# Kernel tuning notes

Hardware: AMD Instinct MI355X
Metric: run time of the kernel (lower is better)

Reference implementation:

```python
import jax, jax.numpy as jnp
import numpy as np

EMBED_DIM = 1024
NUM_HEADS = 16
HEAD_DIM = EMBED_DIM // NUM_HEADS


def setup_inputs() -> dict:
    key = jax.random.key(0)
    ks = jax.random.split(key, 12)
    B, S, D = 4, 2048, EMBED_DIM
    scale = 1.0 / np.sqrt(D)
    inp = {
        "query": jax.random.normal(ks[0], (B, S, D), jnp.float32),
        "key": jax.random.normal(ks[1], (B, S, D), jnp.float32),
        "value": jax.random.normal(ks[2], (B, S, D), jnp.float32),
        # nn.Linear weights: [out_features, in_features], y = x @ W.T + b
        "Wq": jax.random.normal(ks[3], (D, D), jnp.float32) * scale,
        "bq": jnp.zeros((D,), jnp.float32),
        "Wk": jax.random.normal(ks[4], (D, D), jnp.float32) * scale,
        "bk": jnp.zeros((D,), jnp.float32),
        "Wv": jax.random.normal(ks[5], (D, D), jnp.float32) * scale,
        "bv": jnp.zeros((D,), jnp.float32),
        "Wo": jax.random.normal(ks[6], (D, D), jnp.float32) * scale,
        "bo": jnp.zeros((D,), jnp.float32),
    }
    return inp


def reference(query, key, value, Wq, bq, Wk, bk, Wv, bv, Wo, bo):
    B, Sq, D = query.shape
    Sk = key.shape[1]
    H, Dh = NUM_HEADS, HEAD_DIM

    def proj(x, W, b):
        # [B,S,D] -> [B,H,S,Dh]
        y = jnp.einsum('bsd,ed->bse', x, W) + b
        return y.reshape(x.shape[0], x.shape[1], H, Dh).transpose(0, 2, 1, 3)

    q = proj(query, Wq, bq)
    k = proj(key, Wk, bk)
    v = proj(value, Wv, bv)

    # sigmoid attention (no softmax); dropout is identity in eval mode
    scores = jnp.einsum('bhqd,bhkd->bhqk', q, k) / jnp.sqrt(jnp.float32(Dh)).astype(q.dtype)
    attn = jax.nn.sigmoid(scores)
    out = jnp.einsum('bhqk,bhkd->bhqd', attn, v)

    out = out.transpose(0, 2, 1, 3).reshape(B, Sq, D)
    return jnp.einsum('bsd,ed->bse', out, Wo) + bo
```

## Files before the change

kernel.cpp:

```cpp
#include <hip/hip_runtime.h>


typedef _Float16 f16x2 __attribute__((ext_vector_type(2)));
typedef _Float16 f16x4 __attribute__((ext_vector_type(4)));
typedef _Float16 f16x8 __attribute__((ext_vector_type(8)));
typedef __fp16   h16x2 __attribute__((ext_vector_type(2)));
typedef float    f32x4 __attribute__((ext_vector_type(4)));
typedef float    f32x16 __attribute__((ext_vector_type(16)));

typedef __attribute__((address_space(3))) void* lds_vp;
typedef const __attribute__((address_space(1))) void* gbl_vp;

__device__ __forceinline__ void gld_lds16(const void* g, void* l) {
  __builtin_amdgcn_global_load_lds((gbl_vp)g, (lds_vp)l, 16, 0, 0);
}

__device__ __forceinline__ f16x8 cvt8(float4 a, float4 b) {
  return (f16x8){(_Float16)a.x, (_Float16)a.y, (_Float16)a.z, (_Float16)a.w,
                 (_Float16)b.x, (_Float16)b.y, (_Float16)b.z, (_Float16)b.w};
}

__device__ __forceinline__ f16x2 pk2(float a, float b) {
  h16x2 r = __builtin_amdgcn_cvt_pkrtz(a, b);
  return __builtin_bit_cast(f16x2, r);
}

__device__ __forceinline__ float exp2_fast(float x) {
#if __has_builtin(__builtin_amdgcn_exp2f)
  return __builtin_amdgcn_exp2f(x);
#else
  float r;
  asm("v_exp_f32 %0, %1" : "=v"(r) : "v"(x));
  return r;
#endif
}

#define BM 128
#define BN 128
#define BK 32

template <bool AF16, bool BF16, bool TRANSV, bool OUTF32>
__global__ __launch_bounds__(256) void gemm_bt(const void* __restrict__ Av,
                                               const void* __restrict__ Bv,
                                               const float* __restrict__ bias,
                                               void* __restrict__ Yv,
                                               int M, int N, int K) {
  __shared__ __align__(16) _Float16 sA[BM * BK];
  __shared__ __align__(16) _Float16 sB[BN * BK];

  const int t = threadIdx.x, lane = t & 63, wid = t >> 6;
  const int m0 = blockIdx.x * BM, n0 = blockIdx.y * BN;
  const int wm = (wid >> 1) * 64, wn = (wid & 1) * 64;
  const int lrow = lane & 15, g = lane >> 4;

  f32x4 acc[4][4] = {};

  const int arow = 16 * wid + (lane >> 2);
  const int gq = (lane & 3) ^ ((lane >> 3) & 3);
  _Float16* lA1 = sA + wid * 512;
  _Float16* lA2 = sA + 2048 + wid * 512;
  _Float16* lB1 = sB + wid * 512;
  _Float16* lB2 = sB + 2048 + wid * 512;

  const int mrow = t >> 1, mhalf = t & 1;
  const int mm = (mrow >> 1) & 3;
  const int ch_lo = mrow * 4 + ((2 * mhalf) ^ mm);
  const int ch_hi = ch_lo ^ 1;

  const _Float16* pA16a = nullptr; const _Float16* pA16b = nullptr;
  const float* pA32 = nullptr;
  if constexpr (AF16) {
    const _Float16* A = (const _Float16*)Av;
    pA16a = A + (size_t)(m0 + arow) * K + gq * 8;
    pA16b = A + (size_t)(m0 + 64 + arow) * K + gq * 8;
  } else {
    pA32 = (const float*)Av + (size_t)(m0 + mrow) * K + mhalf * 16;
  }
  const _Float16* pB16a = nullptr; const _Float16* pB16b = nullptr;
  const float* pB32 = nullptr;
  if constexpr (BF16) {
    const _Float16* B = (const _Float16*)Bv;
    pB16a = B + (size_t)(n0 + arow) * K + gq * 8;
    pB16b = B + (size_t)(n0 + 64 + arow) * K + gq * 8;
  } else {
    pB32 = (const float*)Bv + (size_t)(n0 + mrow) * K + mhalf * 16;
  }

  const int xr = g ^ ((lrow >> 1) & 3);

  for (int k0 = 0; k0 < K; k0 += BK) {
    float4 av[4], bv4[4];
    if constexpr (!AF16) {
      const float4* p = (const float4*)(pA32 + k0);
      av[0] = p[0]; av[1] = p[1]; av[2] = p[2]; av[3] = p[3];
    }
    if constexpr (!BF16) {
      const float4* p = (const float4*)(pB32 + k0);
      bv4[0] = p[0]; bv4[1] = p[1]; bv4[2] = p[2]; bv4[3] = p[3];
    }
    __syncthreads();
    if constexpr (AF16) {
      gld_lds16(pA16a + k0, lA1);
      gld_lds16(pA16b + k0, lA2);
    } else {
      *(f16x8*)(sA + ch_lo * 8) = cvt8(av[0], av[1]);
      *(f16x8*)(sA + ch_hi * 8) = cvt8(av[2], av[3]);
    }
    if constexpr (BF16) {
      gld_lds16(pB16a + k0, lB1);
      gld_lds16(pB16b + k0, lB2);
    } else {
      *(f16x8*)(sB + ch_lo * 8) = cvt8(bv4[0], bv4[1]);
      *(f16x8*)(sB + ch_hi * 8) = cvt8(bv4[2], bv4[3]);
    }
    __syncthreads();

    f16x8 af[4], bf[4];
#pragma unroll
    for (int i = 0; i < 4; i++)
      af[i] = *(const f16x8*)(sA + (wm + i * 16 + lrow) * 32 + xr * 8);
#pragma unroll
    for (int j = 0; j < 4; j++)
      bf[j] = *(const f16x8*)(sB + (wn + j * 16 + lrow) * 32 + xr * 8);
#pragma unroll
    for (int i = 0; i < 4; i++)
#pragma unroll
      for (int j = 0; j < 4; j++)
        acc[i][j] = __builtin_amdgcn_mfma_f32_16x16x32_f16(af[i], bf[j], acc[i][j], 0, 0, 0);
  }

  const int orow = g * 4, ocol = lrow;
#pragma unroll
  for (int j = 0; j < 4; j++) {
    const int col = n0 + wn + j * 16 + ocol;
    const float bv = bias[col];
#pragma unroll
    for (int i = 0; i < 4; i++) {
      const int row = m0 + wm + i * 16 + orow;
      if constexpr (TRANSV) {
        _Float16* VT = (_Float16*)Yv;
        int s = row & 2047;
        int sp = (s & ~12) | ((s & 4) << 1) | ((s & 8) >> 1);
        _Float16* dst = VT + (((size_t)(row >> 11) * 16 + (col >> 6)) * 64 + (col & 63)) * 2048 + sp;
        f16x4 v = {(_Float16)(acc[i][j][0] + bv), (_Float16)(acc[i][j][1] + bv),
                   (_Float16)(acc[i][j][2] + bv), (_Float16)(acc[i][j][3] + bv)};
        *(f16x4*)dst = v;
      } else if constexpr (OUTF32) {
        float* Y = (float*)Yv;
#pragma unroll
        for (int r = 0; r < 4; r++) Y[(size_t)(row + r) * N + col] = acc[i][j][r] + bv;
      } else {
        _Float16* Y = (_Float16*)Yv;
#pragma unroll
        for (int r = 0; r < 4; r++) Y[(size_t)(row + r) * N + col] = (_Float16)(acc[i][j][r] + bv);
      }
    }
  }
}

__global__ __launch_bounds__(256) void qkv_gemm(const _Float16* __restrict__ Xq,
                                                const _Float16* __restrict__ Xk,
                                                const _Float16* __restrict__ Xv,
                                                const _Float16* __restrict__ W,
                                                const float* __restrict__ bq,
                                                const float* __restrict__ bk,
                                                const float* __restrict__ bv,
                                                _Float16* __restrict__ Qo,
                                                _Float16* __restrict__ Ko,
                                                _Float16* __restrict__ VT) {
  __shared__ __align__(16) _Float16 sA[BM * BK];
  __shared__ __align__(16) _Float16 sB[BN * BK];

  const int t = threadIdx.x, lane = t & 63, wid = t >> 6;
  const int n0g = blockIdx.x * BN, m0 = blockIdx.y * BM;
  const int seg = blockIdx.x >> 3, n0 = n0g & 1023;
  const _Float16* A = (seg == 0) ? Xq : (seg == 1) ? Xk : Xv;
  const float* bias = (seg == 0) ? bq : (seg == 1) ? bk : bv;
  const int K = 1024;

  const int wm = (wid >> 1) * 64, wn = (wid & 1) * 64;
  const int lrow = lane & 15, g = lane >> 4;

  f32x4 acc[4][4] = {};

  const int arow = 16 * wid + (lane >> 2);
  const int gq = (lane & 3) ^ ((lane >> 3) & 3);
  _Float16* lA1 = sA + wid * 512;
  _Float16* lA2 = sA + 2048 + wid * 512;
  _Float16* lB1 = sB + wid * 512;
  _Float16* lB2 = sB + 2048 + wid * 512;

  const _Float16* pA16a = A + (size_t)(m0 + arow) * K + gq * 8;
  const _Float16* pA16b = A + (size_t)(m0 + 64 + arow) * K + gq * 8;
  const _Float16* pB16a = W + (size_t)(n0g + arow) * K + gq * 8;
  const _Float16* pB16b = W + (size_t)(n0g + 64 + arow) * K + gq * 8;

  const int xr = g ^ ((lrow >> 1) & 3);

  for (int k0 = 0; k0 < K; k0 += BK) {
    __syncthreads();
    gld_lds16(pA16a + k0, lA1);
    gld_lds16(pA16b + k0, lA2);
    gld_lds16(pB16a + k0, lB1);
    gld_lds16(pB16b + k0, lB2);
    __syncthreads();

    f16x8 af[4], bf[4];
#pragma unroll
    for (int i = 0; i < 4; i++)
      af[i] = *(const f16x8*)(sA + (wm + i * 16 + lrow) * 32 + xr * 8);
#pragma unroll
    for (int j = 0; j < 4; j++)
      bf[j] = *(const f16x8*)(sB + (wn + j * 16 + lrow) * 32 + xr * 8);
#pragma unroll
    for (int i = 0; i < 4; i++)
#pragma unroll
      for (int j = 0; j < 4; j++)
        acc[i][j] = __builtin_amdgcn_mfma_f32_16x16x32_f16(af[i], bf[j], acc[i][j], 0, 0, 0);
  }

  const int orow = g * 4, ocol = lrow;
#pragma unroll
  for (int j = 0; j < 4; j++) {
    const int col = n0 + wn + j * 16 + ocol;
    const float bvv = bias[col];
#pragma unroll
    for (int i = 0; i < 4; i++) {
      const int row = m0 + wm + i * 16 + orow;
      if (seg == 2) {
        int s = row & 2047;
        int sp = (s & ~12) | ((s & 4) << 1) | ((s & 8) >> 1);
        _Float16* dst = VT + (((size_t)(row >> 11) * 16 + (col >> 6)) * 64 + (col & 63)) * 2048 + sp;
        f16x4 v = {(_Float16)(acc[i][j][0] + bvv), (_Float16)(acc[i][j][1] + bvv),
                   (_Float16)(acc[i][j][2] + bvv), (_Float16)(acc[i][j][3] + bvv)};
        *(f16x4*)dst = v;
      } else {
        _Float16* Y = (seg == 0) ? Qo : Ko;
#pragma unroll
        for (int r = 0; r < 4; r++) Y[(size_t)(row + r) * 1024 + col] = (_Float16)(acc[i][j][r] + bvv);
      }
    }
  }
}

#define LDS_ROW 72
#define TILE_E (64 * LDS_ROW)

__global__ __launch_bounds__(256, 3) void attn_sig(const _Float16* __restrict__ Q,
                                                   const _Float16* __restrict__ K,
                                                   const _Float16* __restrict__ VT,
                                                   _Float16* __restrict__ O) {
  __shared__ __align__(16) _Float16 smem[4 * TILE_E];

  const int t = threadIdx.x, lane = t & 63, wid = t >> 6;
  const int l31 = lane & 31, g5 = lane >> 5;
  const int b = blockIdx.z, h = blockIdx.y, q0 = blockIdx.x * 128;
  const int qw = q0 + wid * 32;
  const int NT = 32;

  f16x8 qf[4];
  {
    const _Float16* qp = Q + (size_t)(b * 2048 + qw + l31) * 1024 + h * 64;
#pragma unroll
    for (int dhc = 0; dhc < 4; dhc++)
      qf[dhc] = *(const f16x8*)(qp + dhc * 16 + g5 * 8) * (_Float16)-0.18033688f;
  }

  f32x16 oacc[2] = {};

  const int srow = t >> 2, scol = (t & 3) * 16;
  const _Float16* kbase = K + ((size_t)(b * 2048) + srow) * 1024 + h * 64 + scol;
  const _Float16* vbase = VT + ((size_t)((b * 16 + h) * 64 + srow)) * 2048 + scol;

#define LOAD_TILE(tile)                                                  \
  ka = *(const uint4*)(kbase + (size_t)(tile) * 64 * 1024);              \
  kb = *(const uint4*)(kbase + (size_t)(tile) * 64 * 1024 + 8);          \
  va = *(const uint4*)(vbase + (tile) * 64);                             \
  vb = *(const uint4*)(vbase + (tile) * 64 + 8);

#define WRITE_TILE(p)                                                    \
  {                                                                      \
    _Float16* dK = smem + (p) * 2 * TILE_E;                              \
    _Float16* dV = dK + TILE_E;                                          \
    *(uint4*)&dK[srow * LDS_ROW + scol] = ka;                            \
    *(uint4*)&dK[srow * LDS_ROW + scol + 8] = kb;                        \
    *(uint4*)&dV[srow * LDS_ROW + scol] = va;                            \
    *(uint4*)&dV[srow * LDS_ROW + scol + 8] = vb;                        \
  }

#define QK_CHUNK(sacc, sKp, c)                                           \
  {                                                                      \
    _Float16* sk_ = (sKp);                                               \
    f16x8 kf0 = *(const f16x8*)&sk_[((c) * 32 + l31) * LDS_ROW + 0 * 16 + g5 * 8];  \
    f16x8 kf1 = *(const f16x8*)&sk_[((c) * 32 + l31) * LDS_ROW + 1 * 16 + g5 * 8];  \
    f16x8 kf2 = *(const f16x8*)&sk_[((c) * 32 + l31) * LDS_ROW + 2 * 16 + g5 * 8];  \
    f16x8 kf3 = *(const f16x8*)&sk_[((c) * 32 + l31) * LDS_ROW + 3 * 16 + g5 * 8];  \
    sacc = __builtin_amdgcn_mfma_f32_32x32x16_f16(kf0, qf[0], sacc, 0, 0, 0);       \
    sacc = __builtin_amdgcn_mfma_f32_32x32x16_f16(kf1, qf[1], sacc, 0, 0, 0);       \
    sacc = __builtin_amdgcn_mfma_f32_32x32x16_f16(kf2, qf[2], sacc, 0, 0, 0);       \
    sacc = __builtin_amdgcn_mfma_f32_32x32x16_f16(kf3, qf[3], sacc, 0, 0, 0);       \
  }

#define PACK_PF(pf, sacc)                                                \
  {                                                                      \
    _Pragma("unroll")                                                    \
    for (int G = 0; G < 2; G++) {                                        \
      union { f16x8 v; f16x2 hh[4]; } u;                                 \
      _Pragma("unroll")                                                  \
      for (int pr = 0; pr < 4; pr++) {                                   \
        float e0 = exp2_fast(sacc[G * 8 + pr * 2 + 0]);                  \
        float e1 = exp2_fast(sacc[G * 8 + pr * 2 + 1]);                  \
        u.hh[pr] = pk2(__builtin_amdgcn_rcpf(1.0f + e0),                 \
                       __builtin_amdgcn_rcpf(1.0f + e1));                \
      }                                                                  \
      pf[G] = u.v;                                                       \
    }                                                                    \
  }

#define VF_READ(vf, sVp, c)                                              \
  {                                                                      \
    _Float16* sv_ = (sVp);                                               \
    vf[0][0] = *(const f16x8*)&sv_[(0 * 32 + l31) * LDS_ROW + (c) * 32 + 0 * 16 + g5 * 8]; \
    vf[0][1] = *(const f16x8*)&sv_[(0 * 32 + l31) * LDS_ROW + (c) * 32 + 1 * 16 + g5 * 8]; \
    vf[1][0] = *(const f16x8*)&sv_[(1 * 32 + l31) * LDS_ROW + (c) * 32 + 0 * 16 + g5 * 8]; \
    vf[1][1] = *(const f16x8*)&sv_[(1 * 32 + l31) * LDS_ROW + (c) * 32 + 1 * 16 + g5 * 8]; \
  }

#define PV_ACC(vf, pf)                                                   \
  oacc[0] = __builtin_amdgcn_mfma_f32_32x32x16_f16(vf[0][0], pf[0], oacc[0], 0, 0, 0); \
  oacc[0] = __builtin_amdgcn_mfma_f32_32x32x16_f16(vf[0][1], pf[1], oacc[0], 0, 0, 0); \
  oacc[1] = __builtin_amdgcn_mfma_f32_32x32x16_f16(vf[1][0], pf[0], oacc[1], 0, 0, 0); \
  oacc[1] = __builtin_amdgcn_mfma_f32_32x32x16_f16(vf[1][1], pf[1], oacc[1], 0, 0, 0);

  uint4 ka, kb, va, vb;
  f16x8 pfA[2], pfP[2];
  f16x8 vfA[2][2], vfP[2][2];
  f32x16 saccA, saccB;

  LOAD_TILE(0);
  WRITE_TILE(0);

  {
    _Float16* sKp = smem;
    _Float16* sVp = smem + TILE_E;
    __syncthreads();
    LOAD_TILE(1);
    saccA = (f32x16){};
    QK_CHUNK(saccA, sKp, 0);
    saccB = (f32x16){};
    QK_CHUNK(saccB, sKp, 1);
    PACK_PF(pfA, saccA);
    VF_READ(vfA, sVp, 0);
    PV_ACC(vfA, pfA);
    PACK_PF(pfP, saccB);
    VF_READ(vfP, sVp, 1);
    WRITE_TILE(1);
  }

  for (int tt = 1; tt < NT; ++tt) {
    const int p = tt & 1;
    _Float16* sKp = smem + p * 2 * TILE_E;
    _Float16* sVp = sKp + TILE_E;
    __syncthreads();
    PV_ACC(vfP, pfP);
    if (tt + 1 < NT) { LOAD_TILE(tt + 1); }
    saccA = (f32x16){};
    QK_CHUNK(saccA, sKp, 0);
    saccB = (f32x16){};
    QK_CHUNK(saccB, sKp, 1);
    PACK_PF(pfA, saccA);
    VF_READ(vfA, sVp, 0);
    PV_ACC(vfA, pfA);
    PACK_PF(pfP, saccB);
    VF_READ(vfP, sVp, 1);
    if (tt + 1 < NT) { WRITE_TILE(p ^ 1); }
  }
  PV_ACC(vfP, pfP);

  __syncthreads();
  _Float16* ep = smem;
#pragma unroll
  for (int dht = 0; dht < 2; dht++)
#pragma unroll
    for (int c = 0; c < 4; c++) {
      f16x4 o4 = {(_Float16)oacc[dht][4 * c + 0], (_Float16)oacc[dht][4 * c + 1],
                  (_Float16)oacc[dht][4 * c + 2], (_Float16)oacc[dht][4 * c + 3]};
      *(f16x4*)&ep[(wid * 32 + l31) * LDS_ROW + dht * 32 + c * 8 + g5 * 4] = o4;
    }
  __syncthreads();
#pragma unroll
  for (int i = 0; i < 4; i++) {
    const int q = i * 32 + (t >> 3), dhc = t & 7;
    f16x8 row = *(const f16x8*)&ep[q * LDS_ROW + dhc * 8];
    *(f16x8*)(O + (size_t)(b * 2048 + q0 + q) * 1024 + h * 64 + dhc * 8) = row;
  }
}

struct CvtArgs {
  const float* src[7];
  _Float16* dst[7];
  int n[7];
  int cnt;
};

__global__ __launch_bounds__(256) void cvt_f32_f16(CvtArgs a) {
  const int ti = blockIdx.y;
  if (ti >= a.cnt) return;
  const int i = (blockIdx.x * 256 + threadIdx.x) * 8;
  if (i >= a.n[ti]) return;
  const float4* s = (const float4*)(a.src[ti] + i);
  float4 x = s[0], y = s[1];
  *(f16x8*)(a.dst[ti] + i) = cvt8(x, y);
}

extern "C" void kernel_launch(void* const* d_in, const int* in_sizes, int n_in,
                              void* d_out, int out_size, void* d_ws, size_t ws_size,
                              hipStream_t stream) {
  const float* query = (const float*)d_in[0];
  const float* key   = (const float*)d_in[1];
  const float* value = (const float*)d_in[2];
  const float* Wq = (const float*)d_in[3];
  const float* bq = (const float*)d_in[4];
  const float* Wk = (const float*)d_in[5];
  const float* bk = (const float*)d_in[6];
  const float* Wv = (const float*)d_in[7];
  const float* bv = (const float*)d_in[8];
  const float* Wo = (const float*)d_in[9];
  const float* bo = (const float*)d_in[10];
  float* out = (float*)d_out;

  const int D = 1024, M = 8192;
  const size_t MB = 1024 * 1024;
  char* ws = (char*)d_ws;
  dim3 bb(256);

  if (ws_size >= 104 * MB) {
    _Float16* Xq = (_Float16*)(ws + 0 * MB);
    _Float16* Xk = (_Float16*)(ws + 16 * MB);
    _Float16* Xv = (_Float16*)(ws + 32 * MB);
    _Float16* Qp = (_Float16*)(ws + 48 * MB);
    _Float16* Kp = (_Float16*)(ws + 64 * MB);
    _Float16* VT = (_Float16*)(ws + 80 * MB);
    _Float16* Wf = (_Float16*)(ws + 96 * MB);
    _Float16* AO = Xq;
    CvtArgs ca{};
    ca.src[0] = query; ca.dst[0] = Xq; ca.n[0] = M * D;
    ca.src[1] = key;   ca.dst[1] = Xk; ca.n[1] = M * D;
    ca.src[2] = value; ca.dst[2] = Xv; ca.n[2] = M * D;
    ca.src[3] = Wq; ca.dst[3] = Wf + 0 * 1048576; ca.n[3] = D * D;
    ca.src[4] = Wk; ca.dst[4] = Wf + 1 * 1048576; ca.n[4] = D * D;
    ca.src[5] = Wv; ca.dst[5] = Wf + 2 * 1048576; ca.n[5] = D * D;
    ca.src[6] = Wo; ca.dst[6] = Wf + 3 * 1048576; ca.n[6] = D * D;
    ca.cnt = 7;
    cvt_f32_f16<<<dim3(4096, 7), bb, 0, stream>>>(ca);
    qkv_gemm<<<dim3(24, 64), bb, 0, stream>>>(Xq, Xk, Xv, Wf, bq, bk, bv, Qp, Kp, VT);
    attn_sig<<<dim3(16, 16, 4), bb, 0, stream>>>(Qp, Kp, VT, AO);
    gemm_bt<true, true, false, true><<<dim3(64, 8), bb, 0, stream>>>(AO, Wf + 3 * 1048576, bo, out, M, D, D);
  } else {
    _Float16* Qp = (_Float16*)(ws + 0 * MB);
    _Float16* Kp = (_Float16*)(ws + 16 * MB);
    _Float16* VT = (_Float16*)(ws + 32 * MB);
    _Float16* AO = (_Float16*)(ws + 48 * MB);
    gemm_bt<false, false, false, false><<<dim3(64, 8), bb, 0, stream>>>(query, Wq, bq, Qp, M, D, D);
    gemm_bt<false, false, false, false><<<dim3(64, 8), bb, 0, stream>>>(key,   Wk, bk, Kp, M, D, D);
    gemm_bt<false, false, true,  false><<<dim3(64, 8), bb, 0, stream>>>(value, Wv, bv, VT, M, D, D);
    attn_sig<<<dim3(16, 16, 4), bb, 0, stream>>>(Qp, Kp, VT, AO);
    gemm_bt<true, false, false, true><<<dim3(64, 8), bb, 0, stream>>>(AO, Wo, bo, out, M, D, D);
  }
}
```

Measured before the change: 370.8 us.

## Double per-wave query rows in sigmoid attention to reuse K/V fragments

```diff
diff --git a/kernel.cpp b/kernel.cpp
--- a/kernel.cpp
+++ b/kernel.cpp
@@ -246,7 +246,7 @@
 #define LDS_ROW 72
 #define TILE_E (64 * LDS_ROW)
 
-__global__ __launch_bounds__(256, 3) void attn_sig(const _Float16* __restrict__ Q,
+__global__ __launch_bounds__(256, 2) void attn_sig(const _Float16* __restrict__ Q,
                                                    const _Float16* __restrict__ K,
                                                    const _Float16* __restrict__ VT,
                                                    _Float16* __restrict__ O) {
@@ -254,19 +254,25 @@
 
   const int t = threadIdx.x, lane = t & 63, wid = t >> 6;
   const int l31 = lane & 31, g5 = lane >> 5;
-  const int b = blockIdx.z, h = blockIdx.y, q0 = blockIdx.x * 128;
-  const int qw = q0 + wid * 32;
+  const int li = (int)(blockIdx.x + 8 * blockIdx.y + 128 * blockIdx.z);
+  const int swz = (li & 7) * 64 + (li >> 3);
+  const int qb = swz & 7, hb = swz >> 3;
+  const int h = hb & 15, b = hb >> 4;
+  const int q0 = qb * 256;
+  const int qw = q0 + wid * 64;
   const int NT = 32;
 
-  f16x8 qf[4];
+  f16x8 qf0[4], qf1[4];
   {
     const _Float16* qp = Q + (size_t)(b * 2048 + qw + l31) * 1024 + h * 64;
 #pragma unroll
-    for (int dhc = 0; dhc < 4; dhc++)
-      qf[dhc] = *(const f16x8*)(qp + dhc * 16 + g5 * 8) * (_Float16)-0.18033688f;
-  }
-
-  f32x16 oacc[2] = {};
+    for (int dhc = 0; dhc < 4; dhc++) {
+      qf0[dhc] = *(const f16x8*)(qp + dhc * 16 + g5 * 8) * (_Float16)-0.18033688f;
+      qf1[dhc] = *(const f16x8*)(qp + 32 * 1024 + dhc * 16 + g5 * 8) * (_Float16)-0.18033688f;
+    }
+  }
+
+  f32x16 oacc00 = {}, oacc01 = {}, oacc10 = {}, oacc11 = {};
 
   const int srow = t >> 2, scol = (t & 3) * 16;
   const _Float16* kbase = K + ((size_t)(b * 2048) + srow) * 1024 + h * 64 + scol;
@@ -286,19 +292,6 @@
     *(uint4*)&dK[srow * LDS_ROW + scol + 8] = kb;                        \
     *(uint4*)&dV[srow * LDS_ROW + scol] = va;                            \
     *(uint4*)&dV[srow * LDS_ROW + scol + 8] = vb;                        \
-  }
-
-#define QK_CHUNK(sacc, sKp, c)                                           \
-  {                                                                      \
-    _Float16* sk_ = (sKp);                                               \
-    f16x8 kf0 = *(const f16x8*)&sk_[((c) * 32 + l31) * LDS_ROW + 0 * 16 + g5 * 8];  \
-    f16x8 kf1 = *(const f16x8*)&sk_[((c) * 32 + l31) * LDS_ROW + 1 * 16 + g5 * 8];  \
-    f16x8 kf2 = *(const f16x8*)&sk_[((c) * 32 + l31) * LDS_ROW + 2 * 16 + g5 * 8];  \
-    f16x8 kf3 = *(const f16x8*)&sk_[((c) * 32 + l31) * LDS_ROW + 3 * 16 + g5 * 8];  \
-    sacc = __builtin_amdgcn_mfma_f32_32x32x16_f16(kf0, qf[0], sacc, 0, 0, 0);       \
-    sacc = __builtin_amdgcn_mfma_f32_32x32x16_f16(kf1, qf[1], sacc, 0, 0, 0);       \
-    sacc = __builtin_amdgcn_mfma_f32_32x32x16_f16(kf2, qf[2], sacc, 0, 0, 0);       \
-    sacc = __builtin_amdgcn_mfma_f32_32x32x16_f16(kf3, qf[3], sacc, 0, 0, 0);       \
   }
 
 #define PACK_PF(pf, sacc)                                                \
@@ -317,83 +310,95 @@
     }                                                                    \
   }
 
-#define VF_READ(vf, sVp, c)                                              \
-  {                                                                      \
-    _Float16* sv_ = (sVp);                                               \
-    vf[0][0] = *(const f16x8*)&sv_[(0 * 32 + l31) * LDS_ROW + (c) * 32 + 0 * 16 + g5 * 8]; \
-    vf[0][1] = *(const f16x8*)&sv_[(0 * 32 + l31) * LDS_ROW + (c) * 32 + 1 * 16 + g5 * 8]; \
-    vf[1][0] = *(const f16x8*)&sv_[(1 * 32 + l31) * LDS_ROW + (c) * 32 + 0 * 16 + g5 * 8]; \
-    vf[1][1] = *(const f16x8*)&sv_[(1 * 32 + l31) * LDS_ROW + (c) * 32 + 1 * 16 + g5 * 8]; \
-  }
-
-#define PV_ACC(vf, pf)                                                   \
-  oacc[0] = __builtin_amdgcn_mfma_f32_32x32x16_f16(vf[0][0], pf[0], oacc[0], 0, 0, 0); \
-  oacc[0] = __builtin_amdgcn_mfma_f32_32x32x16_f16(vf[0][1], pf[1], oacc[0], 0, 0, 0); \
-  oacc[1] = __builtin_amdgcn_mfma_f32_32x32x16_f16(vf[1][0], pf[0], oacc[1], 0, 0, 0); \
-  oacc[1] = __builtin_amdgcn_mfma_f32_32x32x16_f16(vf[1][1], pf[1], oacc[1], 0, 0, 0);
+#define CHUNK(c)                                                                      \
+  {                                                                                   \
+    const _Float16* sk_ = sKp + ((c) * 32 + l31) * LDS_ROW + g5 * 8;                  \
+    f16x8 kf0 = *(const f16x8*)(sk_ + 0);                                             \
+    f16x8 kf1 = *(const f16x8*)(sk_ + 16);                                            \
+    f16x8 kf2 = *(const f16x8*)(sk_ + 32);                                            \
+    f16x8 kf3 = *(const f16x8*)(sk_ + 48);                                            \
+    f32x16 s0 = {}, s1 = {};                                                          \
+    __builtin_amdgcn_s_setprio(1);                                                    \
+    s0 = __builtin_amdgcn_mfma_f32_32x32x16_f16(kf0, qf0[0], s0, 0, 0, 0);            \
+    s1 = __builtin_amdgcn_mfma_f32_32x32x16_f16(kf0, qf1[0], s1, 0, 0, 0);            \
+    s0 = __builtin_amdgcn_mfma_f32_32x32x16_f16(kf1, qf0[1], s0, 0, 0, 0);            \
+    s1 = __builtin_amdgcn_mfma_f32_32x32x16_f16(kf1, qf1[1], s1, 0, 0, 0);            \
+    s0 = __builtin_amdgcn_mfma_f32_32x32x16_f16(kf2, qf0[2], s0, 0, 0, 0);            \
+    s1 = __builtin_amdgcn_mfma_f32_32x32x16_f16(kf2, qf1[2], s1, 0, 0, 0);            \
+    s0 = __builtin_amdgcn_mfma_f32_32x32x16_f16(kf3, qf0[3], s0, 0, 0, 0);            \
+    s1 = __builtin_amdgcn_mfma_f32_32x32x16_f16(kf3, qf1[3], s1, 0, 0, 0);            \
+    __builtin_amdgcn_s_setprio(0);                                                    \
+    f16x8 pf0[2], pf1[2];                                                             \
+    PACK_PF(pf0, s0);                                                                 \
+    PACK_PF(pf1, s1);                                                                 \
+    const _Float16* sv_ = sVp + l31 * LDS_ROW + (c) * 32 + g5 * 8;                    \
+    f16x8 vf00 = *(const f16x8*)(sv_ + 0);                                            \
+    f16x8 vf01 = *(const f16x8*)(sv_ + 16);                                           \
+    f16x8 vf10 = *(const f16x8*)(sv_ + 32 * LDS_ROW);                                 \
+    f16x8 vf11 = *(const f16x8*)(sv_ + 32 * LDS_ROW + 16);                            \
+    __builtin_amdgcn_s_setprio(1);                                                    \
+    oacc00 = __builtin_amdgcn_mfma_f32_32x32x16_f16(vf00, pf0[0], oacc00, 0, 0, 0);   \
+    oacc10 = __builtin_amdgcn_mfma_f32_32x32x16_f16(vf00, pf1[0], oacc10, 0, 0, 0);   \
+    oacc01 = __builtin_amdgcn_mfma_f32_32x32x16_f16(vf10, pf0[0], oacc01, 0, 0, 0);   \
+    oacc11 = __builtin_amdgcn_mfma_f32_32x32x16_f16(vf10, pf1[0], oacc11, 0, 0, 0);   \
+    oacc00 = __builtin_amdgcn_mfma_f32_32x32x16_f16(vf01, pf0[1], oacc00, 0, 0, 0);   \
+    oacc10 = __builtin_amdgcn_mfma_f32_32x32x16_f16(vf01, pf1[1], oacc10, 0, 0, 0);   \
+    oacc01 = __builtin_amdgcn_mfma_f32_32x32x16_f16(vf11, pf0[1], oacc01, 0, 0, 0);   \
+    oacc11 = __builtin_amdgcn_mfma_f32_32x32x16_f16(vf11, pf1[1], oacc11, 0, 0, 0);   \
+    __builtin_amdgcn_s_setprio(0);                                                    \
+  }
 
   uint4 ka, kb, va, vb;
-  f16x8 pfA[2], pfP[2];
-  f16x8 vfA[2][2], vfP[2][2];
-  f32x16 saccA, saccB;
 
   LOAD_TILE(0);
   WRITE_TILE(0);
-
-  {
-    _Float16* sKp = smem;
-    _Float16* sVp = smem + TILE_E;
-    __syncthreads();
-    LOAD_TILE(1);
-    saccA = (f32x16){};
-    QK_CHUNK(saccA, sKp, 0);
-    saccB = (f32x16){};
-    QK_CHUNK(saccB, sKp, 1);
-    PACK_PF(pfA, saccA);
-    VF_READ(vfA, sVp, 0);
-    PV_ACC(vfA, pfA);
-    PACK_PF(pfP, saccB);
-    VF_READ(vfP, sVp, 1);
-    WRITE_TILE(1);
-  }
-
-  for (int tt = 1; tt < NT; ++tt) {
+  LOAD_TILE(1);
+
+  for (int tt = 0; tt < NT; ++tt) {
     const int p = tt & 1;
-    _Float16* sKp = smem + p * 2 * TILE_E;
-    _Float16* sVp = sKp + TILE_E;
-    __syncthreads();
-    PV_ACC(vfP, pfP);
-    if (tt + 1 < NT) { LOAD_TILE(tt + 1); }
-    saccA = (f32x16){};
-    QK_CHUNK(saccA, sKp, 0);
-    saccB = (f32x16){};
-    QK_CHUNK(saccB, sKp, 1);
-    PACK_PF(pfA, saccA);
-    VF_READ(vfA, sVp, 0);
-    PV_ACC(vfA, pfA);
-    PACK_PF(pfP, saccB);
-    VF_READ(vfP, sVp, 1);
+    const _Float16* sKp = smem + p * 2 * TILE_E;
+    const _Float16* sVp = sKp + TILE_E;
+    __syncthreads();
     if (tt + 1 < NT) { WRITE_TILE(p ^ 1); }
-  }
-  PV_ACC(vfP, pfP);
-
-  __syncthreads();
+    if (tt + 2 < NT) { LOAD_TILE(tt + 2); }
+    CHUNK(0);
+    CHUNK(1);
+  }
+
   _Float16* ep = smem;
 #pragma unroll
-  for (int dht = 0; dht < 2; dht++)
-#pragma unroll
-    for (int c = 0; c < 4; c++) {
-      f16x4 o4 = {(_Float16)oacc[dht][4 * c + 0], (_Float16)oacc[dht][4 * c + 1],
-                  (_Float16)oacc[dht][4 * c + 2], (_Float16)oacc[dht][4 * c + 3]};
-      *(f16x4*)&ep[(wid * 32 + l31) * LDS_ROW + dht * 32 + c * 8 + g5 * 4] = o4;
-    }
-  __syncthreads();
-#pragma unroll
-  for (int i = 0; i < 4; i++) {
-    const int q = i * 32 + (t >> 3), dhc = t & 7;
-    f16x8 row = *(const f16x8*)&ep[q * LDS_ROW + dhc * 8];
-    *(f16x8*)(O + (size_t)(b * 2048 + q0 + q) * 1024 + h * 64 + dhc * 8) = row;
-  }
+  for (int pass = 0; pass < 2; pass++) {
+    __syncthreads();
+    if ((wid >> 1) == pass) {
+      const int rbase = (wid & 1) * 64;
+#pragma unroll
+      for (int c = 0; c < 4; c++) {
+        f16x4 a0 = {(_Float16)oacc00[4 * c + 0], (_Float16)oacc00[4 * c + 1],
+                    (_Float16)oacc00[4 * c + 2], (_Float16)oacc00[4 * c + 3]};
+        f16x4 a1 = {(_Float16)oacc01[4 * c + 0], (_Float16)oacc01[4 * c + 1],
+                    (_Float16)oacc01[4 * c + 2], (_Float16)oacc01[4 * c + 3]};
+        *(f16x4*)&ep[(rbase + l31) * LDS_ROW + 0 * 32 + c * 8 + g5 * 4] = a0;
+        *(f16x4*)&ep[(rbase + l31) * LDS_ROW + 1 * 32 + c * 8 + g5 * 4] = a1;
+        f16x4 b0 = {(_Float16)oacc10[4 * c + 0], (_Float16)oacc10[4 * c + 1],
+                    (_Float16)oacc10[4 * c + 2], (_Float16)oacc10[4 * c + 3]};
+        f16x4 b1 = {(_Float16)oacc11[4 * c + 0], (_Float16)oacc11[4 * c + 1],
+                    (_Float16)oacc11[4 * c + 2], (_Float16)oacc11[4 * c + 3]};
+        *(f16x4*)&ep[(rbase + 32 + l31) * LDS_ROW + 0 * 32 + c * 8 + g5 * 4] = b0;
+        *(f16x4*)&ep[(rbase + 32 + l31) * LDS_ROW + 1 * 32 + c * 8 + g5 * 4] = b1;
+      }
+    }
+    __syncthreads();
+#pragma unroll
+    for (int i = 0; i < 4; i++) {
+      const int q = i * 32 + (t >> 3), dhc = t & 7;
+      f16x8 row = *(const f16x8*)&ep[q * LDS_ROW + dhc * 8];
+      *(f16x8*)(O + (size_t)(b * 2048 + q0 + pass * 128 + q) * 1024 + h * 64 + dhc * 8) = row;
+    }
+  }
+#undef LOAD_TILE
+#undef WRITE_TILE
+#undef PACK_PF
+#undef CHUNK
 }
 
 struct CvtArgs {
@@ -454,7 +459,7 @@
     ca.cnt = 7;
     cvt_f32_f16<<<dim3(4096, 7), bb, 0, stream>>>(ca);
     qkv_gemm<<<dim3(24, 64), bb, 0, stream>>>(Xq, Xk, Xv, Wf, bq, bk, bv, Qp, Kp, VT);
-    attn_sig<<<dim3(16, 16, 4), bb, 0, stream>>>(Qp, Kp, VT, AO);
+    attn_sig<<<dim3(8, 16, 4), bb, 0, stream>>>(Qp, Kp, VT, AO);
     gemm_bt<true, true, false, true><<<dim3(64, 8), bb, 0, stream>>>(AO, Wf + 3 * 1048576, bo, out, M, D, D);
   } else {
     _Float16* Qp = (_Float16*)(ws + 0 * MB);
@@ -464,7 +469,7 @@
     gemm_bt<false, false, false, false><<<dim3(64, 8), bb, 0, stream>>>(query, Wq, bq, Qp, M, D, D);
     gemm_bt<false, false, false, false><<<dim3(64, 8), bb, 0, stream>>>(key,   Wk, bk, Kp, M, D, D);
     gemm_bt<false, false, true,  false><<<dim3(64, 8), bb, 0, stream>>>(value, Wv, bv, VT, M, D, D);
-    attn_sig<<<dim3(16, 16, 4), bb, 0, stream>>>(Qp, Kp, VT, AO);
+    attn_sig<<<dim3(8, 16, 4), bb, 0, stream>>>(Qp, Kp, VT, AO);
     gemm_bt<true, false, false, true><<<dim3(64, 8), bb, 0, stream>>>(AO, Wo, bo, out, M, D, D);
   }
 }
```

New measurement: 354.2 us. -4.5%, faster.
